# Kernel optimization log

Hardware: AMD Instinct MI355X
Metric: run time of the kernel (lower is better)

## Reference

```python
import jax, jax.numpy as jnp
import numpy as np

ALPHA, KL, KS = 0.2, 0.3, 1.0  # PGDKernel defaults

_OFFSETS = jnp.array([[a, b, c] for a in (0, 1) for b in (0, 1) for c in (0, 1)], dtype=jnp.int32)  # [8,3]


def _cic_corners(pos, mesh):
    # pos: [N,3] in grid units, periodic wrap
    base = jnp.floor(pos)
    frac = pos - base                              # [N,3]
    base = base.astype(jnp.int32)
    idx = (base[:, None, :] + _OFFSETS[None, :, :]) % mesh   # [N,8,3]
    w = jnp.prod(jnp.where(_OFFSETS[None].astype(bool), frac[:, None, :], 1.0 - frac[:, None, :]), axis=-1)  # [N,8]
    flat = (idx[..., 0] * mesh + idx[..., 1]) * mesh + idx[..., 2]  # [N,8]
    return flat, w


def cic_paint(pos, mesh):
    flat, w = _cic_corners(pos, mesh)
    grid = jnp.zeros((mesh * mesh * mesh,), dtype=pos.dtype)
    grid = grid.at[flat.reshape(-1)].add(w.reshape(-1))
    return grid.reshape(mesh, mesh, mesh)


def cic_read(grid, pos, mesh):
    flat, w = _cic_corners(pos, mesh)
    return jnp.sum(grid.reshape(-1)[flat] * w, axis=-1)  # [N]


def fftk(mesh):
    k = (2.0 * np.pi * jnp.fft.fftfreq(mesh)).astype(jnp.float32)
    return [k.reshape(-1, 1, 1), k.reshape(1, -1, 1), k.reshape(1, 1, -1)]


def setup_inputs() -> dict:
    key = jax.random.key(0)
    k1, k2 = jax.random.split(key)
    mesh = 128
    n = mesh ** 3
    g = jnp.arange(mesh, dtype=jnp.float32)
    lattice = jnp.stack(jnp.meshgrid(g, g, g, indexing='ij'), axis=-1).reshape(-1, 3)
    pos = (lattice + 0.5 * jax.random.normal(k1, (n, 3), dtype=jnp.float32)) % mesh
    vel = 0.01 * jax.random.normal(k2, (n, 3), dtype=jnp.float32)
    return {"pos": pos, "vel": vel, "mesh_size": mesh}


def reference(pos, vel, mesh_size):
    mesh = int(mesh_size)
    delta = cic_paint(pos, mesh)                       # particle-mesh deposit
    delta_k = jnp.fft.fftn(delta)                      # complex64 [m,m,m]
    kvec = fftk(mesh)
    kk = sum(ki ** 2 for ki in kvec)
    kk_safe = jnp.where(kk == 0, 1.0, kk)
    pgd_range = jnp.exp(-(KL ** 2) / kk_safe) * jnp.exp(-(kk ** 2) / (KS ** 4))
    pgd_range = jnp.where(kk == 0, 0.0, pgd_range)
    invlap = -jnp.where(kk == 0, 0.0, 1.0 / kk_safe)   # inverse laplace kernel
    pot_k = delta_k * (invlap * pgd_range)
    # gradient kernel: i*k_i ; force_i = readout(ifft(-grad_i * pot_k))
    forces = jnp.stack(
        [cic_read(jnp.fft.ifftn(-1j * ki * pot_k).real.astype(pos.dtype), pos, mesh) for ki in kvec],
        axis=-1,
    )  # [N,3]
    new_pos = pos + ALPHA * forces
    return new_pos, vel
```

## Files before the change

kernel.cpp:

```cpp
#include <hip/hip_runtime.h>
#include <hip/hip_bf16.h>

#define MESH   128
#define MESH2  16384
#define MESH3  2097152
#define SP 21
#define CELLS (SP * SP * SP)

__device__ __forceinline__ float kfreq(int i) {
    int s = (i < 64) ? i : (i - 128);
    return 0.049087385212340517f * (float)s;
}

__device__ __forceinline__ float load_elem(const void* p, int i, int isbf16) {
    if (isbf16) return __bfloat162float(((const __hip_bfloat16*)p)[i]);
    return ((const float*)p)[i];
}

__device__ __forceinline__ float bf2f(unsigned short u) {
    unsigned int w = ((unsigned int)u) << 16;
    return __uint_as_float(w);
}

__device__ __forceinline__ void ldsAddF(float* p, float v) {
    unsigned off = (unsigned)(unsigned long long)p;
    asm volatile("ds_add_f32 %0, %1" :: "v"(off), "v"(v) : "memory");
}
__device__ __forceinline__ void glbAddF(float* p, float v) {
    asm volatile("global_atomic_add_f32 %0, %1, off" :: "v"(p), "v"(v) : "memory");
}

__device__ __forceinline__ void dft8(float2* a, float sgn) {
    const float r = 0.70710678118654752f;
    float2 b0 = a[0], b1 = a[4], b2 = a[2], b3 = a[6];
    float2 b4 = a[1], b5 = a[5], b6 = a[3], b7 = a[7];
    float2 c0 = make_float2(b0.x + b1.x, b0.y + b1.y);
    float2 c1 = make_float2(b0.x - b1.x, b0.y - b1.y);
    float2 c2 = make_float2(b2.x + b3.x, b2.y + b3.y);
    float2 c3 = make_float2(b2.x - b3.x, b2.y - b3.y);
    float2 c4 = make_float2(b4.x + b5.x, b4.y + b5.y);
    float2 c5 = make_float2(b4.x - b5.x, b4.y - b5.y);
    float2 c6 = make_float2(b6.x + b7.x, b6.y + b7.y);
    float2 c7 = make_float2(b6.x - b7.x, b6.y - b7.y);
    float2 t3 = make_float2(-sgn * c3.y, sgn * c3.x);
    float2 t7 = make_float2(-sgn * c7.y, sgn * c7.x);
    float2 d0 = make_float2(c0.x + c2.x, c0.y + c2.y);
    float2 d2 = make_float2(c0.x - c2.x, c0.y - c2.y);
    float2 d1 = make_float2(c1.x + t3.x, c1.y + t3.y);
    float2 d3 = make_float2(c1.x - t3.x, c1.y - t3.y);
    float2 d4 = make_float2(c4.x + c6.x, c4.y + c6.y);
    float2 d6 = make_float2(c4.x - c6.x, c4.y - c6.y);
    float2 d5 = make_float2(c5.x + t7.x, c5.y + t7.y);
    float2 d7 = make_float2(c5.x - t7.x, c5.y - t7.y);
    float2 w1 = make_float2(r, sgn * r), w3 = make_float2(-r, sgn * r);
    float2 t5 = make_float2(d5.x * w1.x - d5.y * w1.y, d5.x * w1.y + d5.y * w1.x);
    float2 t6 = make_float2(-sgn * d6.y, sgn * d6.x);
    float2 t7b = make_float2(d7.x * w3.x - d7.y * w3.y, d7.x * w3.y + d7.y * w3.x);
    a[0] = make_float2(d0.x + d4.x, d0.y + d4.y);
    a[4] = make_float2(d0.x - d4.x, d0.y - d4.y);
    a[1] = make_float2(d1.x + t5.x, d1.y + t5.y);
    a[5] = make_float2(d1.x - t5.x, d1.y - t5.y);
    a[2] = make_float2(d2.x + t6.x, d2.y + t6.y);
    a[6] = make_float2(d2.x - t6.x, d2.y - t6.y);
    a[3] = make_float2(d3.x + t7b.x, d3.y + t7b.y);
    a[7] = make_float2(d3.x - t7b.x, d3.y - t7b.y);
}

__global__ void detect_kernel(const unsigned int* __restrict__ words,
                              int* __restrict__ flag) {
    int t = threadIdx.x;
    unsigned long long m = __ballot((words[t] >> 15) & 1u);
    if (t == 0) *flag = (__popcll(m) > 16) ? 0 : 1;
}

__global__ __launch_bounds__(1024, 4)
void paint_lds(const void* __restrict__ pos, float* __restrict__ grid,
               const int* __restrict__ flag) {
    __shared__ float tile[CELLS];
    int t = threadIdx.x;
    int bi = blockIdx.x;
    int tz = bi & 7, ty = (bi >> 3) & 7, tx = bi >> 6;
    int x0 = tx * 16, y0 = ty * 16, z0 = tz * 16;
    for (int i = t; i < CELLS; i += 1024) tile[i] = 0.f;
    int isbf16 = *flag;
    __syncthreads();

    int zg = t & 3, dy = (t >> 2) & 15, dx = t >> 6;
    int p0 = (((x0 + dx) << 7) + (y0 + dy)) * 128 + z0 + 4 * zg;

    float P[4][3];
    if (isbf16) {
        const uint2* q = (const uint2*)((const char*)pos + 6ll * p0);
        uint2 a = q[0], b = q[1], c = q[2];
        unsigned int w[6] = {a.x, a.y, b.x, b.y, c.x, c.y};
#pragma unroll
        for (int e = 0; e < 12; ++e) {
            unsigned short h = (e & 1) ? (unsigned short)(w[e >> 1] >> 16)
                                       : (unsigned short)(w[e >> 1] & 0xffffu);
            P[e / 3][e % 3] = bf2f(h);
        }
    } else {
        const float4* q = (const float4*)((const float*)pos + 3ll * p0);
        float4 a = q[0], b = q[1], c = q[2];
        P[0][0] = a.x; P[0][1] = a.y; P[0][2] = a.z;
        P[1][0] = a.w; P[1][1] = b.x; P[1][2] = b.y;
        P[2][0] = b.z; P[2][1] = b.w; P[2][2] = c.x;
        P[3][0] = c.y; P[3][1] = c.z; P[3][2] = c.w;
    }

#pragma unroll
    for (int it = 0; it < 4; ++it) {
        float P0 = P[it][0], P1 = P[it][1], P2 = P[it][2];
        float f0 = floorf(P0), f1 = floorf(P1), f2 = floorf(P2);
        int ix = (int)f0, iy = (int)f1, iz = (int)f2;
        float wx1 = P0 - f0, wy1 = P1 - f1, wz1 = P2 - f2;
        float wx0 = 1.f - wx1, wy0 = 1.f - wy1, wz0 = 1.f - wz1;
        int lx = (ix - x0 + 2) & 127, ly = (iy - y0 + 2) & 127;
        int lz = (iz - z0 + 2) & 127;
        if (lx <= 19 && ly <= 19 && lz <= 19) {
            int b00 = (lx * SP + ly) * SP + lz;
            int b01 = b00 + SP;
            int b10 = b00 + SP * SP;
            int b11 = b10 + SP;
            ldsAddF(&tile[b00],     wx0 * wy0 * wz0);
            ldsAddF(&tile[b00 + 1], wx0 * wy0 * wz1);
            ldsAddF(&tile[b01],     wx0 * wy1 * wz0);
            ldsAddF(&tile[b01 + 1], wx0 * wy1 * wz1);
            ldsAddF(&tile[b10],     wx1 * wy0 * wz0);
            ldsAddF(&tile[b10 + 1], wx1 * wy0 * wz1);
            ldsAddF(&tile[b11],     wx1 * wy1 * wz0);
            ldsAddF(&tile[b11 + 1], wx1 * wy1 * wz1);
        } else {
            int gx = ix & 127, gy = iy & 127, gz = iz & 127;
            int hx = (gx + 1) & 127, hy = (gy + 1) & 127, hz = (gz + 1) & 127;
            glbAddF(&grid[((gx << 7) + gy) * 128 + gz], wx0 * wy0 * wz0);
            glbAddF(&grid[((gx << 7) + gy) * 128 + hz], wx0 * wy0 * wz1);
            glbAddF(&grid[((gx << 7) + hy) * 128 + gz], wx0 * wy1 * wz0);
            glbAddF(&grid[((gx << 7) + hy) * 128 + hz], wx0 * wy1 * wz1);
            glbAddF(&grid[((hx << 7) + gy) * 128 + gz], wx1 * wy0 * wz0);
            glbAddF(&grid[((hx << 7) + gy) * 128 + hz], wx1 * wy0 * wz1);
            glbAddF(&grid[((hx << 7) + hy) * 128 + gz], wx1 * wy1 * wz0);
            glbAddF(&grid[((hx << 7) + hy) * 128 + hz], wx1 * wy1 * wz1);
        }
    }
    __syncthreads();
    for (int i = t; i < CELLS; i += 1024) {
        float v = tile[i];
        if (v != 0.f) {
            int lx = i / (SP * SP);
            int r  = i - lx * (SP * SP);
            int ly = r / SP, lz = r - ly * SP;
            int gx = (x0 - 2 + lx) & 127, gy = (y0 - 2 + ly) & 127;
            int gz = (z0 - 2 + lz) & 127;
            glbAddF(&grid[((gx << 7) + gy) * 128 + gz], v);
        }
    }
}

template<int AXIS, int INV, int LM, int SM>
__global__ __launch_bounds__(256)
void fft8x16(const void* __restrict__ s0, const void* __restrict__ s1,
             void* __restrict__ d0, void* __restrict__ d1, void* __restrict__ d2) {
    __shared__ float2 Z[16 * 137];
    int t = threadIdx.x;
    int l = (AXIS == 2) ? (t >> 4) : (t & 15);
    int u = (AXIS == 2) ? (t & 15) : (t >> 4);
    int L = blockIdx.x * 16 + l;
    int vol = blockIdx.y;
    const float sgn = INV ? 1.f : -1.f;
    const float invN3 = 1.0f / 2097152.0f;
    long base; int es;
    if (AXIS == 2)      { base = (long)L * 128; es = 1; }
    else if (AXIS == 1) { base = (long)(L >> 7) * 16384 + (L & 127); es = 128; }
    else                { base = (long)L; es = 16384; }
    const void* srcv = vol ? s1 : s0;

    float2 v[8];
#pragma unroll
    for (int n1 = 0; n1 < 8; ++n1) {
        int e = 16 * n1 + u;
        if (LM == 1) v[n1] = make_float2(((const float*)srcv)[base + (long)e * es], 0.f);
        else         v[n1] = ((const float2*)srcv)[base + (long)e * es];
    }
    dft8(v, sgn);
#pragma unroll
    for (int k1 = 0; k1 < 8; ++k1) {
        float ang = sgn * 0.049087385212340517f * (float)(u * k1);
        float sn, cs; __sincosf(ang, &sn, &cs);
        float2 y = v[k1];
        Z[l * 137 + k1 * 17 + u] =
            make_float2(y.x * cs - y.y * sn, y.x * sn + y.y * cs);
    }
    __syncthreads();

    int k1 = u & 7, c = u >> 3;
    float2 w[8];
#pragma unroll
    for (int b = 0; b < 8; ++b) {
        float2 za = Z[l * 137 + k1 * 17 + b];
        float2 zb = Z[l * 137 + k1 * 17 + 8 + b];
        float2 s = c ? make_float2(za.x - zb.x, za.y - zb.y)
                     : make_float2(za.x + zb.x, za.y + zb.y);
        if (c && b) {
            float ang = sgn * 0.39269908169872414f * (float)b;
            float sn, cs; __sincosf(ang, &sn, &cs);
            s = make_float2(s.x * cs - s.y * sn, s.x * sn + s.y * cs);
        }
        w[b] = s;
    }
    dft8(w, sgn);
#pragma unroll
    for (int k3 = 0; k3 < 8; ++k3) {
        int k = u + 16 * k3;
        float2 vv = w[k3];
        long idx = base + (long)k * es;
        if (SM == 0) {
            ((float2*)(vol ? d1 : d0))[idx] = vv;
        } else if (SM == 3) {
            float kx = kfreq(k), ky = kfreq(L >> 7), kz = kfreq(L & 127);
            float kk = kx * kx + ky * ky + kz * kz;
            float f = 0.f;
            if (kk > 0.f) f = -__expf(-0.09f / kk - kk * kk) / kk * invN3;
            float a = vv.x * f, b = vv.y * f;
            ((float2*)d0)[idx] = make_float2(-kx * b - ky * a, kx * a - ky * b);
            ((float2*)d1)[idx] = make_float2(-kz * b, kz * a);
        } else {
            if (vol == 0) {
                ((float*)d0)[idx] = vv.x;
                ((float*)d1)[idx] = vv.y;
            } else {
                ((float*)d2)[idx] = vv.x;
            }
        }
    }
}

__global__ __launch_bounds__(256)
void update_pos(const void* __restrict__ pos,
                const float* __restrict__ Fx, const float* __restrict__ Fy,
                const float* __restrict__ Fz, float* __restrict__ out,
                const int* __restrict__ flag, int n) {
    int p = blockIdx.x * blockDim.x + threadIdx.x;
    if (p >= n) return;
    int isbf16 = *flag;
    float P0 = load_elem(pos, 3 * p + 0, isbf16);
    float P1 = load_elem(pos, 3 * p + 1, isbf16);
    float P2 = load_elem(pos, 3 * p + 2, isbf16);
    float f0 = floorf(P0), f1 = floorf(P1), f2 = floorf(P2);
    int ix = ((int)f0) & 127, iy = ((int)f1) & 127, iz = ((int)f2) & 127;
    float wx1 = P0 - f0, wy1 = P1 - f1, wz1 = P2 - f2;
    float wx0 = 1.f - wx1, wy0 = 1.f - wy1, wz0 = 1.f - wz1;
    int jx = (ix + 1) & 127, jy = (iy + 1) & 127, jz = (iz + 1) & 127;
    int b00 = (ix * MESH + iy) * MESH;
    int b01 = (ix * MESH + jy) * MESH;
    int b10 = (jx * MESH + iy) * MESH;
    int b11 = (jx * MESH + jy) * MESH;
    float fx = 0.f, fy = 0.f, fz = 0.f;
    int f; float w;
    f = b00 + iz; w = wx0 * wy0 * wz0; fx += w * Fx[f]; fy += w * Fy[f]; fz += w * Fz[f];
    f = b00 + jz; w = wx0 * wy0 * wz1; fx += w * Fx[f]; fy += w * Fy[f]; fz += w * Fz[f];
    f = b01 + iz; w = wx0 * wy1 * wz0; fx += w * Fx[f]; fy += w * Fy[f]; fz += w * Fz[f];
    f = b01 + jz; w = wx0 * wy1 * wz1; fx += w * Fx[f]; fy += w * Fy[f]; fz += w * Fz[f];
    f = b10 + iz; w = wx1 * wy0 * wz0; fx += w * Fx[f]; fy += w * Fy[f]; fz += w * Fz[f];
    f = b10 + jz; w = wx1 * wy0 * wz1; fx += w * Fx[f]; fy += w * Fy[f]; fz += w * Fz[f];
    f = b11 + iz; w = wx1 * wy1 * wz0; fx += w * Fx[f]; fy += w * Fy[f]; fz += w * Fz[f];
    f = b11 + jz; w = wx1 * wy1 * wz1; fx += w * Fx[f]; fy += w * Fy[f]; fz += w * Fz[f];
    out[3 * p + 0] = P0 + 0.2f * fx;
    out[3 * p + 1] = P1 + 0.2f * fy;
    out[3 * p + 2] = P2 + 0.2f * fz;
}

__global__ __launch_bounds__(256)
void copy_vel(const void* __restrict__ vel, float* __restrict__ dst,
              const int* __restrict__ flag, int m) {
    int i0 = (blockIdx.x * blockDim.x + threadIdx.x) * 4;
    int isbf16 = *flag;
#pragma unroll
    for (int j = 0; j < 4; ++j) {
        int i = i0 + j;
        if (i < m) dst[i] = load_elem(vel, i, isbf16);
    }
}

extern "C" void kernel_launch(void* const* d_in, const int* in_sizes, int n_in,
                              void* d_out, int out_size, void* d_ws, size_t ws_size,
                              hipStream_t stream) {
    int n = in_sizes[0] / 3;
    const void* pos = d_in[0];
    const void* vel = d_in[1];
    float* out = (float*)d_out;

    char* ws = (char*)d_ws;
    int*    flag = (int*)ws;
    float2* A  = (float2*)(ws + 4096);
    float*  F0 = (float*)(ws + 4096 + (16u << 20));
    float*  F1 = (float*)(ws + 4096 + (24u << 20));
    float*  delta = (float*)d_out;
    float2* G2 = (float2*)((char*)d_out + (24u << 20));
    float*  F2 = (float*)((char*)d_out + (40u << 20));

    detect_kernel<<<1, 64, 0, stream>>>((const unsigned int*)pos, flag);
    hipMemsetAsync(delta, 0, MESH3 * sizeof(float), stream);
    paint_lds<<<512, 1024, 0, stream>>>(pos, delta, flag);

    fft8x16<2, 0, 1, 0><<<dim3(1024, 1), 256, 0, stream>>>(delta, nullptr, A, nullptr, nullptr);
    fft8x16<1, 0, 0, 0><<<dim3(1024, 1), 256, 0, stream>>>(A, nullptr, A, nullptr, nullptr);
    fft8x16<0, 0, 0, 3><<<dim3(1024, 1), 256, 0, stream>>>(A, nullptr, A, G2, nullptr);

    fft8x16<2, 1, 0, 0><<<dim3(1024, 2), 256, 0, stream>>>(A, G2, A, G2, nullptr);
    fft8x16<1, 1, 0, 0><<<dim3(1024, 2), 256, 0, stream>>>(A, G2, A, G2, nullptr);
    fft8x16<0, 1, 0, 4><<<dim3(1024, 2), 256, 0, stream>>>(A, G2, F0, F1, F2);

    update_pos<<<(n + 255) / 256, 256, 0, stream>>>(pos, F0, F1, F2, out, flag, n);
    int m = 3 * n;
    copy_vel<<<(m / 4 + 255) / 256, 256, 0, stream>>>(vel, out + m, flag, m);
}
```

Baseline: 297.9 us.

## Replace atomic tile flush with per-block scratch dump and gather kernel

Each paint block now writes its full padded LDS tile to a per-block scratch region in workspace instead of atomically adding non-zero cells into the global grid. A new flush_gather kernel then computes each grid cell by summing its own tile entry and up to seven halo contributions from neighbouring tiles, without atomics. This removes global atomic contention on the tile flush but adds an extra kernel launch and about 19 MB of scratch traffic. Particles that take the global-atomic fallback path still add into the grid, which the gather then adds to with +=.

```diff
diff --git a/kernel.cpp b/kernel.cpp
--- a/kernel.cpp
+++ b/kernel.cpp
@@ -6,6 +6,7 @@
 #define MESH3  2097152
 #define SP 21
 #define CELLS (SP * SP * SP)
+#define TSTRIDE 9264
 
 __device__ __forceinline__ float kfreq(int i) {
     int s = (i < 64) ? i : (i - 128);
@@ -75,13 +76,13 @@
 
 __global__ __launch_bounds__(1024, 4)
 void paint_lds(const void* __restrict__ pos, float* __restrict__ grid,
-               const int* __restrict__ flag) {
-    __shared__ float tile[CELLS];
+               float* __restrict__ scratch, const int* __restrict__ flag) {
+    __shared__ __align__(16) float tile[TSTRIDE];
     int t = threadIdx.x;
     int bi = blockIdx.x;
     int tz = bi & 7, ty = (bi >> 3) & 7, tx = bi >> 6;
     int x0 = tx * 16, y0 = ty * 16, z0 = tz * 16;
-    for (int i = t; i < CELLS; i += 1024) tile[i] = 0.f;
+    for (int i = t; i < TSTRIDE; i += 1024) tile[i] = 0.f;
     int isbf16 = *flag;
     __syncthreads();
 
@@ -144,17 +145,42 @@
         }
     }
     __syncthreads();
-    for (int i = t; i < CELLS; i += 1024) {
-        float v = tile[i];
-        if (v != 0.f) {
-            int lx = i / (SP * SP);
-            int r  = i - lx * (SP * SP);
-            int ly = r / SP, lz = r - ly * SP;
-            int gx = (x0 - 2 + lx) & 127, gy = (y0 - 2 + ly) & 127;
-            int gz = (z0 - 2 + lz) & 127;
-            glbAddF(&grid[((gx << 7) + gy) * 128 + gz], v);
-        }
-    }
+    const float4* tf = (const float4*)tile;
+    float4* sf = (float4*)scratch + (size_t)bi * (TSTRIDE / 4);
+    for (int j = t; j < TSTRIDE / 4; j += 1024) sf[j] = tf[j];
+}
+
+__global__ __launch_bounds__(256)
+void flush_gather(const float* __restrict__ scratch, float* __restrict__ grid) {
+    int c = blockIdx.x * 256 + threadIdx.x;
+    int gz = c & 127, gy = (c >> 7) & 127, gx = c >> 14;
+    int tx = gx >> 4, mx = gx & 15;
+    int ty = gy >> 4, my = gy & 15;
+    int tz = gz >> 4, mz = gz & 15;
+    int lx = mx + 2, ly = my + 2, lz = mz + 2;
+    bool hx = (mx < 3) | (mx > 13);
+    bool hy = (my < 3) | (my > 13);
+    bool hz = (mz < 3) | (mz > 13);
+    int t1x = (mx < 3) ? ((tx + 7) & 7) : ((tx + 1) & 7);
+    int l1x = (mx < 3) ? (mx + 18) : (mx - 14);
+    int t1y = (my < 3) ? ((ty + 7) & 7) : ((ty + 1) & 7);
+    int l1y = (my < 3) ? (my + 18) : (my - 14);
+    int t1z = (mz < 3) ? ((tz + 7) & 7) : ((tz + 1) & 7);
+    int l1z = (mz < 3) ? (mz + 18) : (mz - 14);
+
+#define RD(a, la, b, lb, d, ld) \
+    scratch[(size_t)(((a) << 6) + ((b) << 3) + (d)) * TSTRIDE + ((la) * SP + (lb)) * SP + (ld)]
+
+    float s = RD(tx, lx, ty, ly, tz, lz);
+    if (hz)           s += RD(tx, lx, ty, ly, t1z, l1z);
+    if (hy)           s += RD(tx, lx, t1y, l1y, tz, lz);
+    if (hy && hz)     s += RD(tx, lx, t1y, l1y, t1z, l1z);
+    if (hx)           s += RD(t1x, l1x, ty, ly, tz, lz);
+    if (hx && hz)     s += RD(t1x, l1x, ty, ly, t1z, l1z);
+    if (hx && hy)     s += RD(t1x, l1x, t1y, l1y, tz, lz);
+    if (hx && hy && hz) s += RD(t1x, l1x, t1y, l1y, t1z, l1z);
+#undef RD
+    grid[c] += s;
 }
 
 template<int AXIS, int INV, int LM, int SM>
@@ -292,6 +318,7 @@
 
     char* ws = (char*)d_ws;
     int*    flag = (int*)ws;
+    float*  scratch = (float*)(ws + 4096);
     float2* A  = (float2*)(ws + 4096);
     float*  F0 = (float*)(ws + 4096 + (16u << 20));
     float*  F1 = (float*)(ws + 4096 + (24u << 20));
@@ -301,7 +328,8 @@
 
     detect_kernel<<<1, 64, 0, stream>>>((const unsigned int*)pos, flag);
     hipMemsetAsync(delta, 0, MESH3 * sizeof(float), stream);
-    paint_lds<<<512, 1024, 0, stream>>>(pos, delta, flag);
+    paint_lds<<<512, 1024, 0, stream>>>(pos, delta, scratch, flag);
+    flush_gather<<<MESH3 / 256, 256, 0, stream>>>(scratch, delta);
 
     fft8x16<2, 0, 1, 0><<<dim3(1024, 1), 256, 0, stream>>>(delta, nullptr, A, nullptr, nullptr);
     fft8x16<1, 0, 0, 0><<<dim3(1024, 1), 256, 0, stream>>>(A, nullptr, A, nullptr, nullptr);
```

New measurement: 306.3 us. 1.03x slower.

## Fuse 3D FFT passes into plane-in-LDS kernels and fused x-axis round trip

Applied to the files above, without the earlier changes.

Replaces six per-axis FFT launches with three kernels: a forward kernel that holds a full 128x128 plane in LDS and does the z and y FFTs, a kernel that does the forward x FFT, applies the PGD/gradient kernel and runs the inverse x FFTs for both output volumes, and an inverse kernel doing the y and z FFTs per plane. This cuts global memory round trips for the intermediate complex volumes. The cost is large LDS use per block (about 132KB), which limits occupancy, and only 128 or 256 blocks for the plane kernels.

```diff
diff --git a/kernel.cpp b/kernel.cpp
--- a/kernel.cpp
+++ b/kernel.cpp
@@ -6,6 +6,7 @@
 #define MESH3  2097152
 #define SP 21
 #define CELLS (SP * SP * SP)
+#define PSTR 129
 
 __device__ __forceinline__ float kfreq(int i) {
     int s = (i < 64) ? i : (i - 128);
@@ -66,6 +67,74 @@
     a[7] = make_float2(d3.x - t7b.x, d3.y - t7b.y);
 }
 
+__device__ __forceinline__ void fft128_plane(float2* pl, int lb, int stride,
+                                             int u, float sgn) {
+    float2 v[8];
+#pragma unroll
+    for (int n1 = 0; n1 < 8; ++n1) v[n1] = pl[lb + (16 * n1 + u) * stride];
+    dft8(v, sgn);
+#pragma unroll
+    for (int k1 = 0; k1 < 8; ++k1) {
+        float ang = sgn * 0.049087385212340517f * (float)(u * k1);
+        float sn, cs; __sincosf(ang, &sn, &cs);
+        float2 y = v[k1];
+        int slot = k1 * 16 + ((u + 2 * k1) & 15);
+        pl[lb + slot * stride] = make_float2(y.x * cs - y.y * sn, y.x * sn + y.y * cs);
+    }
+    asm volatile("" ::: "memory");
+    int k1 = u & 7, c = u >> 3;
+    float2 w[8];
+#pragma unroll
+    for (int b = 0; b < 8; ++b) {
+        float2 za = pl[lb + (k1 * 16 + ((b + 2 * k1) & 15)) * stride];
+        float2 zb = pl[lb + (k1 * 16 + ((8 + b + 2 * k1) & 15)) * stride];
+        float2 s = c ? make_float2(za.x - zb.x, za.y - zb.y)
+                     : make_float2(za.x + zb.x, za.y + zb.y);
+        if (c && b) {
+            float ang = sgn * 0.39269908169872414f * (float)b;
+            float sn, cs; __sincosf(ang, &sn, &cs);
+            s = make_float2(s.x * cs - s.y * sn, s.x * sn + s.y * cs);
+        }
+        w[b] = s;
+    }
+    dft8(w, sgn);
+    asm volatile("" ::: "memory");
+#pragma unroll
+    for (int k3 = 0; k3 < 8; ++k3) pl[lb + (u + 16 * k3) * stride] = w[k3];
+}
+
+__device__ __forceinline__ void fft128_Z(float2* Z, int l, int u, float sgn,
+                                         float2* v) {
+    __syncthreads();
+    dft8(v, sgn);
+#pragma unroll
+    for (int k1 = 0; k1 < 8; ++k1) {
+        float ang = sgn * 0.049087385212340517f * (float)(u * k1);
+        float sn, cs; __sincosf(ang, &sn, &cs);
+        float2 y = v[k1];
+        Z[l * 137 + k1 * 17 + u] = make_float2(y.x * cs - y.y * sn, y.x * sn + y.y * cs);
+    }
+    __syncthreads();
+    int k1 = u & 7, c = u >> 3;
+    float2 w[8];
+#pragma unroll
+    for (int b = 0; b < 8; ++b) {
+        float2 za = Z[l * 137 + k1 * 17 + b];
+        float2 zb = Z[l * 137 + k1 * 17 + 8 + b];
+        float2 s = c ? make_float2(za.x - zb.x, za.y - zb.y)
+                     : make_float2(za.x + zb.x, za.y + zb.y);
+        if (c && b) {
+            float ang = sgn * 0.39269908169872414f * (float)b;
+            float sn, cs; __sincosf(ang, &sn, &cs);
+            s = make_float2(s.x * cs - s.y * sn, s.x * sn + s.y * cs);
+        }
+        w[b] = s;
+    }
+    dft8(w, sgn);
+#pragma unroll
+    for (int k3 = 0; k3 < 8; ++k3) v[k3] = w[k3];
+}
+
 __global__ void detect_kernel(const unsigned int* __restrict__ words,
                               int* __restrict__ flag) {
     int t = threadIdx.x;
@@ -157,81 +226,97 @@
     }
 }
 
-template<int AXIS, int INV, int LM, int SM>
+__global__ __launch_bounds__(1024)
+void fft_zy_fwd(const float* __restrict__ delta, float2* __restrict__ A) {
+    __shared__ float2 pl[128 * PSTR];
+    int t = threadIdx.x, x = blockIdx.x;
+    const float4* src = (const float4*)(delta + (long)x * MESH2);
+    for (int i = t; i < MESH2 / 4; i += 1024) {
+        float4 d = src[i];
+        int y = i >> 5, z0 = (i & 31) * 4;
+        float2* row = &pl[y * PSTR + z0];
+        row[0] = make_float2(d.x, 0.f); row[1] = make_float2(d.y, 0.f);
+        row[2] = make_float2(d.z, 0.f); row[3] = make_float2(d.w, 0.f);
+    }
+    __syncthreads();
+    int u = t & 15, ln = t >> 4;
+    fft128_plane(pl, ln * PSTR, 1, u, -1.f);
+    fft128_plane(pl, (ln + 64) * PSTR, 1, u, -1.f);
+    __syncthreads();
+    fft128_plane(pl, ln, PSTR, u, -1.f);
+    fft128_plane(pl, ln + 64, PSTR, u, -1.f);
+    __syncthreads();
+    float4* dst = (float4*)(A + (long)x * MESH2);
+    for (int i = t; i < MESH2 / 2; i += 1024) {
+        int y = i >> 6, z0 = (i & 63) * 2;
+        float2 e0 = pl[y * PSTR + z0], e1 = pl[y * PSTR + z0 + 1];
+        dst[i] = make_float4(e0.x, e0.y, e1.x, e1.y);
+    }
+}
+
 __global__ __launch_bounds__(256)
-void fft8x16(const void* __restrict__ s0, const void* __restrict__ s1,
-             void* __restrict__ d0, void* __restrict__ d1, void* __restrict__ d2) {
+void fft_x_fused(float2* __restrict__ A, float2* __restrict__ G2) {
     __shared__ float2 Z[16 * 137];
     int t = threadIdx.x;
-    int l = (AXIS == 2) ? (t >> 4) : (t & 15);
-    int u = (AXIS == 2) ? (t & 15) : (t >> 4);
+    int l = t & 15, u = t >> 4;
     int L = blockIdx.x * 16 + l;
-    int vol = blockIdx.y;
-    const float sgn = INV ? 1.f : -1.f;
     const float invN3 = 1.0f / 2097152.0f;
-    long base; int es;
-    if (AXIS == 2)      { base = (long)L * 128; es = 1; }
-    else if (AXIS == 1) { base = (long)(L >> 7) * 16384 + (L & 127); es = 128; }
-    else                { base = (long)L; es = 16384; }
-    const void* srcv = vol ? s1 : s0;
-
-    float2 v[8];
-#pragma unroll
-    for (int n1 = 0; n1 < 8; ++n1) {
-        int e = 16 * n1 + u;
-        if (LM == 1) v[n1] = make_float2(((const float*)srcv)[base + (long)e * es], 0.f);
-        else         v[n1] = ((const float2*)srcv)[base + (long)e * es];
-    }
-    dft8(v, sgn);
-#pragma unroll
-    for (int k1 = 0; k1 < 8; ++k1) {
-        float ang = sgn * 0.049087385212340517f * (float)(u * k1);
-        float sn, cs; __sincosf(ang, &sn, &cs);
-        float2 y = v[k1];
-        Z[l * 137 + k1 * 17 + u] =
-            make_float2(y.x * cs - y.y * sn, y.x * sn + y.y * cs);
-    }
-    __syncthreads();
-
-    int k1 = u & 7, c = u >> 3;
-    float2 w[8];
-#pragma unroll
-    for (int b = 0; b < 8; ++b) {
-        float2 za = Z[l * 137 + k1 * 17 + b];
-        float2 zb = Z[l * 137 + k1 * 17 + 8 + b];
-        float2 s = c ? make_float2(za.x - zb.x, za.y - zb.y)
-                     : make_float2(za.x + zb.x, za.y + zb.y);
-        if (c && b) {
-            float ang = sgn * 0.39269908169872414f * (float)b;
-            float sn, cs; __sincosf(ang, &sn, &cs);
-            s = make_float2(s.x * cs - s.y * sn, s.x * sn + s.y * cs);
-        }
-        w[b] = s;
-    }
-    dft8(w, sgn);
+    float2 X[8];
+#pragma unroll
+    for (int n1 = 0; n1 < 8; ++n1) X[n1] = A[(long)(16 * n1 + u) * MESH2 + L];
+    fft128_Z(Z, l, u, -1.f, X);
+    float ky = kfreq(L >> 7), kz = kfreq(L & 127);
+    float2 g1[8], g2[8];
 #pragma unroll
     for (int k3 = 0; k3 < 8; ++k3) {
         int k = u + 16 * k3;
-        float2 vv = w[k3];
-        long idx = base + (long)k * es;
-        if (SM == 0) {
-            ((float2*)(vol ? d1 : d0))[idx] = vv;
-        } else if (SM == 3) {
-            float kx = kfreq(k), ky = kfreq(L >> 7), kz = kfreq(L & 127);
-            float kk = kx * kx + ky * ky + kz * kz;
-            float f = 0.f;
-            if (kk > 0.f) f = -__expf(-0.09f / kk - kk * kk) / kk * invN3;
-            float a = vv.x * f, b = vv.y * f;
-            ((float2*)d0)[idx] = make_float2(-kx * b - ky * a, kx * a - ky * b);
-            ((float2*)d1)[idx] = make_float2(-kz * b, kz * a);
-        } else {
-            if (vol == 0) {
-                ((float*)d0)[idx] = vv.x;
-                ((float*)d1)[idx] = vv.y;
-            } else {
-                ((float*)d2)[idx] = vv.x;
-            }
-        }
+        float kx = kfreq(k);
+        float kk = kx * kx + ky * ky + kz * kz;
+        float f = 0.f;
+        if (kk > 0.f) f = -__expf(-0.09f / kk - kk * kk) / kk * invN3;
+        float a = X[k3].x * f, b = X[k3].y * f;
+        g1[k3] = make_float2(-kx * b - ky * a, kx * a - ky * b);
+        g2[k3] = make_float2(-kz * b, kz * a);
+    }
+    fft128_Z(Z, l, u, 1.f, g1);
+#pragma unroll
+    for (int k3 = 0; k3 < 8; ++k3) A[(long)(u + 16 * k3) * MESH2 + L] = g1[k3];
+    fft128_Z(Z, l, u, 1.f, g2);
+#pragma unroll
+    for (int k3 = 0; k3 < 8; ++k3) G2[(long)(u + 16 * k3) * MESH2 + L] = g2[k3];
+}
+
+__global__ __launch_bounds__(1024)
+void fft_yz_inv(const float2* __restrict__ G1, const float2* __restrict__ G2,
+                float* __restrict__ F0, float* __restrict__ F1,
+                float* __restrict__ F2) {
+    __shared__ float2 pl[128 * PSTR];
+    int t = threadIdx.x, x = blockIdx.x, vol = blockIdx.y;
+    const float4* src = (const float4*)((vol ? G2 : G1) + (long)x * MESH2);
+    for (int i = t; i < MESH2 / 2; i += 1024) {
+        float4 d = src[i];
+        int y = i >> 6, z0 = (i & 63) * 2;
+        pl[y * PSTR + z0]     = make_float2(d.x, d.y);
+        pl[y * PSTR + z0 + 1] = make_float2(d.z, d.w);
+    }
+    __syncthreads();
+    int u = t & 15, ln = t >> 4;
+    fft128_plane(pl, ln * PSTR, 1, u, 1.f);
+    fft128_plane(pl, (ln + 64) * PSTR, 1, u, 1.f);
+    __syncthreads();
+    fft128_plane(pl, ln, PSTR, u, 1.f);
+    fft128_plane(pl, ln + 64, PSTR, u, 1.f);
+    __syncthreads();
+    long b = (long)x * MESH2;
+    if (vol == 0) {
+        for (int i = t; i < MESH2; i += 1024) {
+            float2 v = pl[(i >> 7) * PSTR + (i & 127)];
+            F0[b + i] = v.x;
+            F1[b + i] = v.y;
+        }
+    } else {
+        for (int i = t; i < MESH2; i += 1024)
+            F2[b + i] = pl[(i >> 7) * PSTR + (i & 127)].x;
     }
 }
 
@@ -303,13 +388,9 @@
     hipMemsetAsync(delta, 0, MESH3 * sizeof(float), stream);
     paint_lds<<<512, 1024, 0, stream>>>(pos, delta, flag);
 
-    fft8x16<2, 0, 1, 0><<<dim3(1024, 1), 256, 0, stream>>>(delta, nullptr, A, nullptr, nullptr);
-    fft8x16<1, 0, 0, 0><<<dim3(1024, 1), 256, 0, stream>>>(A, nullptr, A, nullptr, nullptr);
-    fft8x16<0, 0, 0, 3><<<dim3(1024, 1), 256, 0, stream>>>(A, nullptr, A, G2, nullptr);
-
-    fft8x16<2, 1, 0, 0><<<dim3(1024, 2), 256, 0, stream>>>(A, G2, A, G2, nullptr);
-    fft8x16<1, 1, 0, 0><<<dim3(1024, 2), 256, 0, stream>>>(A, G2, A, G2, nullptr);
-    fft8x16<0, 1, 0, 4><<<dim3(1024, 2), 256, 0, stream>>>(A, G2, F0, F1, F2);
+    fft_zy_fwd<<<128, 1024, 0, stream>>>(delta, A);
+    fft_x_fused<<<1024, 256, 0, stream>>>(A, G2);
+    fft_yz_inv<<<dim3(128, 2), 1024, 0, stream>>>(A, G2, F0, F1, F2);
 
     update_pos<<<(n + 255) / 256, 256, 0, stream>>>(pos, F0, F1, F2, out, flag, n);
     int m = 3 * n;
```

New measurement: 290.5 us. 1.03x faster.
